# Optimization experiments

Hardware: AMD Instinct MI355X
Metric: run time of the kernel (lower is better)

Reference implementation:

```python
import jax, jax.numpy as jnp
import numpy as np

N_NODES = 100000
N_EDGES = 1600000
N_GRAPHS = 2048
HID = 64
IN_F = 14
N_CLS = 2
EPS = 1e-5


def _gcn_conv(x, row, col, w_edge, W, b, n_nodes):
    # PyG GCNConv with add_self_loops=True, normalize=True.
    xw = x @ W  # [N, out]
    # degree on target nodes, self-loop contributes weight 1
    deg = jnp.zeros((n_nodes,), x.dtype).at[col].add(w_edge) + 1.0
    dinv = deg ** -0.5
    norm = dinv[row] * w_edge * dinv[col]  # [E]
    out = jnp.zeros_like(xw).at[col].add(norm[:, None] * xw[row])
    out = out + (dinv * dinv)[:, None] * xw  # self-loop term
    return out + b


def _bn_relu(x, gamma, beta):
    mean = jnp.mean(x, axis=0)
    var = jnp.var(x, axis=0)  # biased, as PyTorch BN training normalization
    y = gamma * (x - mean) * jax.lax.rsqrt(var + EPS) + beta
    return jax.nn.relu(y)


def setup_inputs() -> dict:
    key = jax.random.key(0)
    ks = jax.random.split(key, 8)
    x = jax.random.normal(ks[0], (N_NODES, IN_F), dtype=jnp.float32)
    edge_index = jax.random.randint(ks[1], (2, N_EDGES), 0, N_NODES, dtype=jnp.int64)
    batch = jnp.sort(jax.random.randint(ks[2], (N_NODES,), 0, N_GRAPHS, dtype=jnp.int64))
    edge_weight = jnp.ones((N_EDGES,), dtype=jnp.float32)
    def lin(k, fi, fo):
        s = 1.0 / np.sqrt(fi)
        kw, kb = jax.random.split(k)
        return (jax.random.uniform(kw, (fi, fo), jnp.float32, -s, s),
                jax.random.uniform(kb, (fo,), jnp.float32, -s, s))
    W1, b1 = lin(ks[3], IN_F, HID)
    W2, b2 = lin(ks[4], HID, HID)
    W3, b3 = lin(ks[5], HID, HID)
    fcW, fcb = lin(ks[6], HID, N_CLS)
    g = jnp.ones((HID,), jnp.float32)
    z = jnp.zeros((HID,), jnp.float32)
    return {
        "x": x, "edge_index": edge_index, "batch": batch, "edge_weight": edge_weight,
        "W1": W1, "b1": b1, "W2": W2, "b2": b2, "W3": W3, "b3": b3,
        "g1": g, "bt1": z, "g2": g, "bt2": z, "g3": g, "bt3": z,
        "fcW": fcW, "fcb": fcb,
    }


def reference(x, edge_index, batch, edge_weight, W1, b1, W2, b2, W3, b3,
              g1, bt1, g2, bt2, g3, bt3, fcW, fcb):
    row, col = edge_index[0], edge_index[1]
    n = x.shape[0]
    h = _bn_relu(_gcn_conv(x, row, col, edge_weight, W1, b1, n), g1, bt1)
    h = _bn_relu(_gcn_conv(h, row, col, edge_weight, W2, b2, n), g2, bt2)
    h = _bn_relu(_gcn_conv(h, row, col, edge_weight, W3, b3, n), g3, bt3)
    node_embs = h  # dropout p=0 is identity
    graph_emb = jax.ops.segment_sum(node_embs, batch, num_segments=N_GRAPHS)
    out = graph_emb @ fcW + fcb
    return (out, node_embs, graph_emb)
```

## Files before the change

kernel.cpp:

```cpp
#include <hip/hip_runtime.h>
#include <hip/hip_fp16.h>

#define N_NODES 100000
#define N_EDGES 1600000
#define EMAX2   1700000
#define N_GRAPHS 2048
#define HID 64
#define IN_F 14
#define N_CLS 2
#define EPS 1e-5f

#define BSHIFT 9
#define NBUCK 196
#define ABLOCKS 256
#define CHUNK (N_EDGES / ABLOCKS)

#define NBLK2 128
#define NCHUNK2 ((N_NODES + NBLK2 - 1) / NBLK2)

typedef _Float16 half_t;
typedef _Float16 half8 __attribute__((ext_vector_type(8)));
typedef float f32x4 __attribute__((ext_vector_type(4)));

#define GSTRIDE ((size_t)N_NODES * 16)


__global__ __launch_bounds__(256) void histA_kernel(const int* __restrict__ col,
                                                    int* __restrict__ histG) {
    __shared__ int hl[NBUCK];
    for (int i = threadIdx.x; i < NBUCK; i += 256) hl[i] = 0;
    __syncthreads();
    int e0 = blockIdx.x * CHUNK;
    for (int e = e0 + threadIdx.x; e < e0 + CHUNK; e += 256)
        atomicAdd(&hl[col[e] >> BSHIFT], 1);
    __syncthreads();
    for (int i = threadIdx.x; i < NBUCK; i += 256)
        histG[i * ABLOCKS + blockIdx.x] = hl[i];
}

__global__ __launch_bounds__(256) void scanS1_kernel(const int* __restrict__ histG,
                                                     int* __restrict__ bsumA) {
    __shared__ int ls[256];
    ls[threadIdx.x] = histG[blockIdx.x * 256 + threadIdx.x];
    __syncthreads();
    for (int off = 128; off > 0; off >>= 1) {
        if (threadIdx.x < off) ls[threadIdx.x] += ls[threadIdx.x + off];
        __syncthreads();
    }
    if (threadIdx.x == 0) bsumA[blockIdx.x] = ls[0];
}

__global__ __launch_bounds__(512) void topscan_kernel(int* __restrict__ bsum, int nb) {
    __shared__ int ls[512];
    int t = threadIdx.x;
    int v = (t < nb) ? bsum[t] : 0;
    ls[t] = v;
    __syncthreads();
    for (int off = 1; off < 512; off <<= 1) {
        int x = ls[t];
        if (t >= off) x += ls[t - off];
        __syncthreads();
        ls[t] = x;
        __syncthreads();
    }
    if (t < nb) bsum[t] = ls[t] - v;
}

__global__ __launch_bounds__(256) void scanS3_kernel(int* __restrict__ histG,
                                                     const int* __restrict__ bsumA,
                                                     int* __restrict__ ptr) {
    __shared__ int ls[256];
    int idx = blockIdx.x * 256 + threadIdx.x;
    int v = histG[idx];
    ls[threadIdx.x] = v;
    __syncthreads();
    for (int off = 1; off < 256; off <<= 1) {
        int x = ls[threadIdx.x];
        if (threadIdx.x >= off) x += ls[threadIdx.x - off];
        __syncthreads();
        ls[threadIdx.x] = x;
        __syncthreads();
    }
    histG[idx] = ls[threadIdx.x] - v + bsumA[blockIdx.x];
    if (blockIdx.x == 0 && threadIdx.x == 0) ptr[N_NODES] = N_EDGES;
}

__global__ __launch_bounds__(256) void scatterA_kernel(const int* __restrict__ row,
                                                       const int* __restrict__ col,
                                                       const float* __restrict__ w,
                                                       const int* __restrict__ histG,
                                                       int2* __restrict__ EA) {
    __shared__ int cur[NBUCK];
    for (int i = threadIdx.x; i < NBUCK; i += 256)
        cur[i] = histG[i * ABLOCKS + blockIdx.x];
    __syncthreads();
    int e0 = blockIdx.x * CHUNK;
    for (int e = e0 + threadIdx.x; e < e0 + CHUNK; e += 256) {
        int c = col[e];
        int r = row[e];
        int fx = (int)__float2uint_rn(w[e] * 8192.0f);
        int pos = atomicAdd(&cur[c >> BSHIFT], 1);
        EA[pos] = make_int2(r, (fx << 17) | c);
    }
}

__global__ __launch_bounds__(256) void bucketA_kernel(const int2* __restrict__ EA,
                                                      const int* __restrict__ bsumA,
                                                      int* __restrict__ ptr,
                                                      float* __restrict__ dinv) {
    __shared__ int hist[512], wsum[512];
    int b = blockIdx.x;
    int beg = bsumA[b];
    int end = (b == NBUCK - 1) ? N_EDGES : bsumA[b + 1];
    int i0 = threadIdx.x, i1 = threadIdx.x + 256;
    hist[i0] = 0; hist[i1] = 0;
    wsum[i0] = 0; wsum[i1] = 0;
    __syncthreads();
    for (int e = beg + threadIdx.x; e < end; e += 256) {
        int2 ed = EA[e];
        int c9 = ed.y & 511;
        atomicAdd(&hist[c9], 1);
        atomicAdd(&wsum[c9], (int)((unsigned int)ed.y >> 17));
    }
    __syncthreads();
    int cnt0 = hist[i0], cnt1 = hist[i1];
    for (int off = 1; off < 512; off <<= 1) {
        int v0 = hist[i0], v1 = hist[i1];
        int a0 = (i0 >= off) ? hist[i0 - off] : 0;
        int a1 = (i1 >= off) ? hist[i1 - off] : 0;
        __syncthreads();
        hist[i0] = v0 + a0;
        hist[i1] = v1 + a1;
        __syncthreads();
    }
    int excl0 = hist[i0] - cnt0, excl1 = hist[i1] - cnt1;
    int col0 = (b << BSHIFT) + i0, col1 = (b << BSHIFT) + i1;
    if (col0 < N_NODES) {
        ptr[col0] = beg + excl0;
        dinv[col0] = rsqrtf(1.0f + (float)wsum[i0] * (1.0f / 8192.0f));
    }
    if (col1 < N_NODES) {
        ptr[col1] = beg + excl1;
        dinv[col1] = rsqrtf(1.0f + (float)wsum[i1] * (1.0f / 8192.0f));
    }
}


__global__ __launch_bounds__(256) void histD_kernel(const int* __restrict__ ptr,
                                                    int* __restrict__ histD) {
    __shared__ int hl[2048];
    for (int i = threadIdx.x; i < 2048; i += 256) hl[i] = 0;
    __syncthreads();
    int n0 = blockIdx.x * NCHUNK2;
    int n1 = n0 + NCHUNK2; if (n1 > N_NODES) n1 = N_NODES;
    for (int n = n0 + threadIdx.x; n < n1; n += 256) {
        int d = ptr[n + 1] - ptr[n];
        if (d > 255) d = 255;
        atomicAdd(&hl[((threadIdx.x & 7) << 8) + d], 1);
    }
    __syncthreads();
    int s = 0;
#pragma unroll
    for (int c = 0; c < 8; c++) s += hl[(c << 8) + threadIdx.x];
    histD[threadIdx.x * NBLK2 + blockIdx.x] = s;
}

__global__ __launch_bounds__(128) void scanD1_kernel(const int* __restrict__ histD,
                                                     int* __restrict__ rowTot) {
    __shared__ int ls[128];
    ls[threadIdx.x] = histD[blockIdx.x * NBLK2 + threadIdx.x];
    __syncthreads();
    for (int off = 64; off > 0; off >>= 1) {
        if (threadIdx.x < off) ls[threadIdx.x] += ls[threadIdx.x + off];
        __syncthreads();
    }
    if (threadIdx.x == 0) rowTot[blockIdx.x] = ls[0];
}

__global__ __launch_bounds__(256) void topscanD_kernel(const int* __restrict__ rowTot,
                                                       int* __restrict__ nodeExcl,
                                                       int* __restrict__ edgeExcl,
                                                       int* __restrict__ ptrS) {
    __shared__ int a[256], b[256];
    int t = threadIdx.x;
    int cnt = rowTot[t];
    int dpad = (t + 1) & ~1;
    int ec = cnt * dpad;
    a[t] = cnt; b[t] = ec;
    __syncthreads();
    for (int off = 1; off < 256; off <<= 1) {
        int va = a[t], vb = b[t];
        if (t >= off) { va += a[t - off]; vb += b[t - off]; }
        __syncthreads();
        a[t] = va; b[t] = vb;
        __syncthreads();
    }
    nodeExcl[t] = a[t] - cnt;
    edgeExcl[t] = b[t] - ec;
    if (t == 255) ptrS[N_NODES] = b[255];
}

__global__ __launch_bounds__(128) void scanD3_kernel(int* __restrict__ histD,
                                                     const int* __restrict__ nodeExcl) {
    __shared__ int ls[128];
    int idx = blockIdx.x * NBLK2 + threadIdx.x;
    int v = histD[idx];
    ls[threadIdx.x] = v;
    __syncthreads();
    for (int off = 1; off < 128; off <<= 1) {
        int x = ls[threadIdx.x];
        if (threadIdx.x >= off) x += ls[threadIdx.x - off];
        __syncthreads();
        ls[threadIdx.x] = x;
        __syncthreads();
    }
    histD[idx] = ls[threadIdx.x] - v + nodeExcl[blockIdx.x];
}

__global__ __launch_bounds__(256) void scatterD_kernel(const int* __restrict__ ptr,
                                                       const int* __restrict__ histD,
                                                       const int* __restrict__ nodeExcl,
                                                       const int* __restrict__ edgeExcl,
                                                       int* __restrict__ perm,
                                                       int* __restrict__ ptrS,
                                                       int* __restrict__ newbase) {
    __shared__ int cur[256];
    cur[threadIdx.x] = histD[threadIdx.x * NBLK2 + blockIdx.x];
    __syncthreads();
    int n0 = blockIdx.x * NCHUNK2;
    int n1 = n0 + NCHUNK2; if (n1 > N_NODES) n1 = N_NODES;
    for (int n = n0 + threadIdx.x; n < n1; n += 256) {
        int d = ptr[n + 1] - ptr[n];
        if (d > 255) d = 255;
        int dpad = (d + 1) & ~1;
        int pos = atomicAdd(&cur[d], 1);
        int ebase = edgeExcl[d] + (pos - nodeExcl[d]) * dpad;
        perm[pos] = n;
        ptrS[pos] = ebase;
        newbase[n] = ebase;
    }
}

__global__ __launch_bounds__(256) void bucketB_kernel(const int2* __restrict__ EA,
                                                      const int* __restrict__ bsumA,
                                                      const int* __restrict__ newbase,
                                                      const float* __restrict__ dinv,
                                                      unsigned int* __restrict__ srcoff,
                                                      half_t* __restrict__ normh) {
    __shared__ int cur[512];
    int b = blockIdx.x;
    int beg = bsumA[b];
    int end = (b == NBUCK - 1) ? N_EDGES : bsumA[b + 1];
    int i0 = threadIdx.x, i1 = threadIdx.x + 256;
    int col0 = (b << BSHIFT) + i0, col1 = (b << BSHIFT) + i1;
    cur[i0] = (col0 < N_NODES) ? newbase[col0] : 0;
    cur[i1] = (col1 < N_NODES) ? newbase[col1] : 0;
    __syncthreads();
    for (int e = beg + threadIdx.x; e < end; e += 256) {
        int2 ed = EA[e];
        int c = ed.y & 0x1ffff;
        float w = (float)((unsigned int)ed.y >> 17) * (1.0f / 8192.0f);
        float nrm = dinv[ed.x] * w * dinv[c];
        int pos = atomicAdd(&cur[c & 511], 1);
        srcoff[pos] = (unsigned int)ed.x << 5;
        normh[pos] = (half_t)nrm;
    }
}


template <int K>
__global__ __launch_bounds__(256) void gemm_kernel(const float* __restrict__ h,
                                                   const float* __restrict__ W,
                                                   half_t* __restrict__ xw, int n_nodes) {
    int f = threadIdx.x & 63;
    float wcol[K];
#pragma unroll
    for (int k = 0; k < K; k++) wcol[k] = W[k * HID + f];
    half_t* xg = xw + (size_t)(f >> 4) * GSTRIDE + (f & 15);
    int wave = (blockIdx.x * blockDim.x + threadIdx.x) >> 6;
    int nwaves = (gridDim.x * blockDim.x) >> 6;
    for (int n = wave; n < n_nodes; n += nwaves) {
        const float* hr = h + (size_t)n * K;
        float acc = 0.f;
#pragma unroll
        for (int k = 0; k < K; k++) acc += hr[k] * wcol[k];
        xg[(size_t)n * 16] = (half_t)acc;
    }
}

__global__ __launch_bounds__(256) void gemm_bn_mfma_kernel(const half_t* __restrict__ h,
                                                           const float* __restrict__ W,
                                                           const float* __restrict__ stats,
                                                           const float* __restrict__ gamma,
                                                           const float* __restrict__ beta,
                                                           half_t* __restrict__ xw, int n_nodes) {
    __shared__ float sc_s[HID], sh_s[HID];
    if (threadIdx.x < 64) {
        float mean = stats[threadIdx.x] * (1.0f / N_NODES);
        float var = stats[64 + threadIdx.x] * (1.0f / N_NODES) - mean * mean;
        float sc = gamma[threadIdx.x] * rsqrtf(var + EPS);
        sc_s[threadIdx.x] = sc;
        sh_s[threadIdx.x] = beta[threadIdx.x] - mean * sc;
    }
    __syncthreads();
    int lane = threadIdx.x & 63;
    int col16 = lane & 15;
    int quad = lane >> 4;

    float scA[2][8], shA[2][8];
#pragma unroll
    for (int kh = 0; kh < 2; kh++)
#pragma unroll
        for (int j = 0; j < 8; j++) {
            int k = kh * 32 + quad * 8 + j;
            scA[kh][j] = sc_s[k];
            shA[kh][j] = sh_s[k];
        }

    half8 bfrag[4][2];
#pragma unroll
    for (int t = 0; t < 4; t++)
#pragma unroll
        for (int kh = 0; kh < 2; kh++)
#pragma unroll
            for (int j = 0; j < 8; j++) {
                int k = kh * 32 + quad * 8 + j;
                bfrag[t][kh][j] = (half_t)W[k * HID + t * 16 + col16];
            }

    int wave = (blockIdx.x * blockDim.x + threadIdx.x) >> 6;
    int nwaves = (gridDim.x * blockDim.x) >> 6;
    int ntiles = n_nodes >> 4;
    for (int tIdx = wave; tIdx < ntiles; tIdx += nwaves) {
        int n0 = tIdx << 4;
        half8 afrag[2];
#pragma unroll
        for (int kh = 0; kh < 2; kh++) {
            int k0 = kh * 32 + quad * 8;
            const half_t* hp = h + (size_t)(k0 >> 4) * GSTRIDE
                                 + (size_t)(n0 + col16) * 16 + (k0 & 15);
            half8 raw = *(const half8*)hp;
#pragma unroll
            for (int j = 0; j < 8; j++) {
                float v = (float)raw[j] * scA[kh][j] + shA[kh][j];
                afrag[kh][j] = (half_t)fmaxf(v, 0.f);
            }
        }
        f32x4 acc[4];
#pragma unroll
        for (int t = 0; t < 4; t++) {
            f32x4 z = {0.f, 0.f, 0.f, 0.f};
            acc[t] = __builtin_amdgcn_mfma_f32_16x16x32_f16(afrag[0], bfrag[t][0], z, 0, 0, 0);
            acc[t] = __builtin_amdgcn_mfma_f32_16x16x32_f16(afrag[1], bfrag[t][1], acc[t], 0, 0, 0);
        }
#pragma unroll
        for (int t = 0; t < 4; t++) {
            half_t* xg = xw + (size_t)t * GSTRIDE;
#pragma unroll
            for (int r = 0; r < 4; r++) {
                int rowi = n0 + quad * 4 + r;
                xg[(size_t)rowi * 16 + col16] = (half_t)acc[t][r];
            }
        }
    }
}

__global__ __launch_bounds__(256) void gather_stats_kernel(const int* __restrict__ ptrS,
                                                           const int* __restrict__ perm,
                                                           const unsigned int* __restrict__ srcoff,
                                                           const unsigned int* __restrict__ normu,
                                                           const half_t* __restrict__ xw,
                                                           const float* __restrict__ dinv,
                                                           const float* __restrict__ b,
                                                           half_t* __restrict__ hp,
                                                           float* __restrict__ stats,
                                                           int n_nodes) {
    int g = (blockIdx.x & 7) >> 1;
    int grank = ((blockIdx.x >> 3) << 1) | (blockIdx.x & 1);
    int lane16 = threadIdx.x & 15;
    int quadLocal = threadIdx.x >> 4;
    int quadId = grank * 16 + quadLocal;
    int nquads = (gridDim.x >> 2) * 16;

    const half_t* xg = xw + (size_t)g * GSTRIDE;
    const char* xgc = (const char*)xg;
    unsigned int loff = (unsigned int)(lane16 * 2);
    half_t* hpg = hp + (size_t)g * GSTRIDE;
    int f = g * 16 + lane16;
    float bf = b[f];
    int base = ((threadIdx.x & 63) >> 4) * 16;

    float s = 0.f, s2 = 0.f;

    int i = quadId;
    int node = 0, beg = 0, c = 0;
    int ev = 0, nv = 0;
    if (i < n_nodes) {
        node = perm[i];
        beg = ptrS[i];
        c = ptrS[i + 1] - beg;
        int m = (c > 16) ? 16 : c;
        if (lane16 < m) ev = (int)srcoff[beg + lane16];
        if (lane16 < (m >> 1)) nv = (int)normu[(beg >> 1) + lane16];
    }

    while (i < n_nodes) {
        int inext = i + nquads;
        int node2 = 0, beg2 = 0, c2 = 0;
        if (inext < n_nodes) {
            node2 = perm[inext];
            beg2 = ptrS[inext];
            c2 = ptrS[inext + 1] - beg2;
        }
        float selfv = (float)xg[(size_t)node * 16 + lane16];
        float di = dinv[node];

        __half2 acc0 = __float2half2_rn(0.f);
        __half2 acc1 = __float2half2_rn(0.f);
        for (int j0 = 0; j0 < c; j0 += 16) {
            int m = c - j0;
            if (m > 16) m = 16;
            int pairs = m >> 1;
            int ev2 = 0, nv2 = 0;
            int j1 = j0 + 16;
            if (j1 < c) {
                int m2 = c - j1;
                if (m2 > 16) m2 = 16;
                if (lane16 < m2) ev2 = (int)srcoff[beg + j1 + lane16];
                if (lane16 < (m2 >> 1)) nv2 = (int)normu[((beg + j1) >> 1) + lane16];
            }
            int p = 0;
            for (; p + 2 <= pairs; p += 2) {
                unsigned int u0 = (unsigned int)__shfl(ev, base + 2 * p);
                unsigned int u1 = (unsigned int)__shfl(ev, base + 2 * p + 1);
                unsigned int u2 = (unsigned int)__shfl(ev, base + 2 * p + 2);
                unsigned int u3 = (unsigned int)__shfl(ev, base + 2 * p + 3);
                unsigned int nd0 = (unsigned int)__shfl(nv, base + p);
                unsigned int nd1 = (unsigned int)__shfl(nv, base + p + 1);
                __half h0 = *(const __half*)(xgc + (u0 + loff));
                __half h1 = *(const __half*)(xgc + (u1 + loff));
                __half h2 = *(const __half*)(xgc + (u2 + loff));
                __half h3 = *(const __half*)(xgc + (u3 + loff));
                __half2 n01 = *(__half2*)&nd0;
                __half2 n23 = *(__half2*)&nd1;
                acc0 = __hfma2(n01, __halves2half2(h0, h1), acc0);
                acc1 = __hfma2(n23, __halves2half2(h2, h3), acc1);
            }
            if (p < pairs) {
                unsigned int u0 = (unsigned int)__shfl(ev, base + 2 * p);
                unsigned int u1 = (unsigned int)__shfl(ev, base + 2 * p + 1);
                unsigned int nd0 = (unsigned int)__shfl(nv, base + p);
                __half h0 = *(const __half*)(xgc + (u0 + loff));
                __half h1 = *(const __half*)(xgc + (u1 + loff));
                __half2 n01 = *(__half2*)&nd0;
                acc0 = __hfma2(n01, __halves2half2(h0, h1), acc0);
            }
            ev = ev2; nv = nv2;
        }
        if (inext < n_nodes) {
            int m = (c2 > 16) ? 16 : c2;
            ev = (lane16 < m) ? (int)srcoff[beg2 + lane16] : 0;
            nv = (lane16 < (m >> 1)) ? (int)normu[(beg2 >> 1) + lane16] : 0;
        }

        float accf = (__low2float(acc0) + __high2float(acc0))
                   + (__low2float(acc1) + __high2float(acc1));
        float v = accf + di * di * selfv + bf;
        hpg[(size_t)node * 16 + lane16] = (half_t)v;
        s += v;
        s2 += v * v;

        i = inext; node = node2; beg = beg2; c = c2;
    }
    __shared__ float ls[256], ls2[256];
    ls[threadIdx.x] = s;
    ls2[threadIdx.x] = s2;
    __syncthreads();
    if (threadIdx.x < 16) {
        float a = 0.f, aa = 0.f;
#pragma unroll
        for (int k = 0; k < 16; k++) {
            a += ls[k * 16 + threadIdx.x];
            aa += ls2[k * 16 + threadIdx.x];
        }
        atomicAdd(&stats[g * 16 + threadIdx.x], a);
        atomicAdd(&stats[64 + g * 16 + threadIdx.x], aa);
    }
}

__global__ __launch_bounds__(256) void bn_relu_seg_kernel(const half_t* __restrict__ hpl,
                                                          float* __restrict__ h3,
                                                          const float* __restrict__ stats,
                                                          const float* __restrict__ gamma,
                                                          const float* __restrict__ beta,
                                                          const int* __restrict__ batch,
                                                          float* __restrict__ gemb,
                                                          int n_nodes) {
    int g = blockIdx.x * blockDim.x + threadIdx.x;
    int f = g & 63;
    int wave = g >> 6;
    int nwaves = (gridDim.x * blockDim.x) >> 6;
    int chunk = (n_nodes + nwaves - 1) / nwaves;
    int n0 = wave * chunk;
    int n1 = n0 + chunk;
    if (n1 > n_nodes) n1 = n_nodes;
    if (n0 >= n_nodes) return;
    float mean = stats[f] * (1.0f / N_NODES);
    float var = stats[64 + f] * (1.0f / N_NODES) - mean * mean;
    float sc = gamma[f] * rsqrtf(var + EPS);
    float sh = beta[f] - mean * sc;
    const half_t* hg = hpl + (size_t)(f >> 4) * GSTRIDE + (f & 15);
    int curg = batch[n0];
    float racc = 0.f;
    for (int n = n0; n < n1; n++) {
        int bg = batch[n];
        if (bg != curg) {
            atomicAdd(&gemb[(size_t)curg * HID + f], racc);
            racc = 0.f;
            curg = bg;
        }
        float v = (float)hg[(size_t)n * 16] * sc + sh;
        v = fmaxf(v, 0.f);
        h3[(size_t)n * HID + f] = v;
        racc += v;
    }
    atomicAdd(&gemb[(size_t)curg * HID + f], racc);
}

__global__ __launch_bounds__(256) void final_kernel(const float* __restrict__ gemb,
                                                    const float* __restrict__ fcW,
                                                    const float* __restrict__ fcb,
                                                    float* __restrict__ out) {
    int g = blockIdx.x * blockDim.x + threadIdx.x;
    if (g >= N_GRAPHS * N_CLS) return;
    int gr = g >> 1, c = g & 1;
    float acc = fcb[c];
#pragma unroll
    for (int k = 0; k < HID; k++) acc += gemb[gr * HID + k] * fcW[k * N_CLS + c];
    out[g] = acc;
}


extern "C" void kernel_launch(void* const* d_in, const int* in_sizes, int n_in,
                              void* d_out, int out_size, void* d_ws, size_t ws_size,
                              hipStream_t stream) {
    const float* x    = (const float*)d_in[0];
    const int*   ei   = (const int*)d_in[1];
    const int*   batch= (const int*)d_in[2];
    const float* ew   = (const float*)d_in[3];
    const float* W1   = (const float*)d_in[4];
    const float* b1   = (const float*)d_in[5];
    const float* W2   = (const float*)d_in[6];
    const float* b2   = (const float*)d_in[7];
    const float* W3   = (const float*)d_in[8];
    const float* b3   = (const float*)d_in[9];
    const float* g1   = (const float*)d_in[10];
    const float* bt1  = (const float*)d_in[11];
    const float* g2   = (const float*)d_in[12];
    const float* bt2  = (const float*)d_in[13];
    const float* g3   = (const float*)d_in[14];
    const float* bt3  = (const float*)d_in[15];
    const float* fcW  = (const float*)d_in[16];
    const float* fcb  = (const float*)d_in[17];

    const int* row = ei;
    const int* col = ei + N_EDGES;

    float* out_head  = (float*)d_out;
    float* node_embs = out_head + N_GRAPHS * N_CLS;
    float* gemb      = node_embs + (size_t)N_NODES * HID;

    char* bse = (char*)d_ws;
    half_t* xwh = (half_t*)bse;
    char* r1 = bse + (size_t)N_NODES * HID * 2;
    int2*   EA  = (int2*)r1;
    half_t* hpl = (half_t*)r1;
    char* r2 = r1 + (size_t)N_NODES * HID * 2;
    unsigned int* srcoff = (unsigned int*)r2;
    half_t* normh = (half_t*)(srcoff + EMAX2);
    char* r3 = r2 + (size_t)EMAX2 * 6;
    float* dinv  = (float*)r3;
    float* stats3 = dinv + N_NODES;
    int*   ptr   = (int*)(stats3 + 384);
    int*   histG = ptr + N_NODES + 1;
    int*   bsumA = histG + NBUCK * ABLOCKS;
    int*   histD = bsumA + NBUCK + 4;
    int*   rowTot = histD + 256 * NBLK2;
    int*   nodeExcl = rowTot + 256;
    int*   edgeExcl = nodeExcl + 256;
    int*   perm   = edgeExcl + 256;
    int*   newbase= perm + N_NODES;
    int*   ptrS   = newbase + N_NODES;

    const int B   = 256;
    const int gGS = 1024;
    const int gGA = 2048;

    hipMemsetAsync(srcoff, 0, (size_t)EMAX2 * 6, stream);
    hipMemsetAsync(stats3, 0, 384 * sizeof(float), stream);
    hipMemsetAsync(gemb, 0, (size_t)N_GRAPHS * HID * sizeof(float), stream);

    histA_kernel<<<ABLOCKS, B, 0, stream>>>(col, histG);
    scanS1_kernel<<<NBUCK, B, 0, stream>>>(histG, bsumA);
    topscan_kernel<<<1, 512, 0, stream>>>(bsumA, NBUCK);
    scanS3_kernel<<<NBUCK, B, 0, stream>>>(histG, bsumA, ptr);
    scatterA_kernel<<<ABLOCKS, B, 0, stream>>>(row, col, ew, histG, EA);
    bucketA_kernel<<<NBUCK, B, 0, stream>>>(EA, bsumA, ptr, dinv);

    histD_kernel<<<NBLK2, B, 0, stream>>>(ptr, histD);
    scanD1_kernel<<<256, 128, 0, stream>>>(histD, rowTot);
    topscanD_kernel<<<1, 256, 0, stream>>>(rowTot, nodeExcl, edgeExcl, ptrS);
    scanD3_kernel<<<256, 128, 0, stream>>>(histD, nodeExcl);
    scatterD_kernel<<<NBLK2, B, 0, stream>>>(ptr, histD, nodeExcl, edgeExcl,
                                             perm, ptrS, newbase);
    bucketB_kernel<<<NBUCK, B, 0, stream>>>(EA, bsumA, newbase, dinv, srcoff, normh);

    float* h3 = node_embs;

    gemm_kernel<IN_F><<<gGS, B, 0, stream>>>(x, W1, xwh, N_NODES);
    gather_stats_kernel<<<gGA, B, 0, stream>>>(ptrS, perm, srcoff,
                                               (const unsigned int*)normh, xwh,
                                               dinv, b1, hpl, stats3, N_NODES);

    gemm_bn_mfma_kernel<<<gGS, B, 0, stream>>>(hpl, W2, stats3, g1, bt1, xwh, N_NODES);
    gather_stats_kernel<<<gGA, B, 0, stream>>>(ptrS, perm, srcoff,
                                               (const unsigned int*)normh, xwh,
                                               dinv, b2, hpl, stats3 + 128, N_NODES);

    gemm_bn_mfma_kernel<<<gGS, B, 0, stream>>>(hpl, W3, stats3 + 128, g2, bt2, xwh, N_NODES);
    gather_stats_kernel<<<gGA, B, 0, stream>>>(ptrS, perm, srcoff,
                                               (const unsigned int*)normh, xwh,
                                               dinv, b3, hpl, stats3 + 256, N_NODES);

    bn_relu_seg_kernel<<<gGS, B, 0, stream>>>(hpl, h3, stats3 + 256, g3, bt3,
                                              batch, gemb, N_NODES);

    final_kernel<<<(N_GRAPHS * N_CLS + B - 1) / B, B, 0, stream>>>(gemb, fcW, fcb, out_head);
}
```

Measured before the change: 407.6 us.

## Pad CSR edge lists to multiples of four and load indices as vectors

Per-node edge segments are now padded to a multiple of four instead of two, with the edge buffer capacity raised to match. The aggregation kernel then drops the cooperative shuffle-based broadcast of source offsets and norms, and has each lane read them directly with uint4/uint2 vector loads. This removes shuffle instructions and the prefetch logic, but increases padded edge storage and issues redundant broadcast loads across the 16 lanes of each node group. It also loses the software prefetch of the next node's indices.

```diff
diff --git a/kernel.cpp b/kernel.cpp
--- a/kernel.cpp
+++ b/kernel.cpp
@@ -3,7 +3,7 @@
 
 #define N_NODES 100000
 #define N_EDGES 1600000
-#define EMAX2   1700000
+#define EMAX2   2000000
 #define N_GRAPHS 2048
 #define HID 64
 #define IN_F 14
@@ -184,7 +184,7 @@
     __shared__ int a[256], b[256];
     int t = threadIdx.x;
     int cnt = rowTot[t];
-    int dpad = (t + 1) & ~1;
+    int dpad = (t + 3) & ~3;
     int ec = cnt * dpad;
     a[t] = cnt; b[t] = ec;
     __syncthreads();
@@ -232,7 +232,7 @@
     for (int n = n0 + threadIdx.x; n < n1; n += 256) {
         int d = ptr[n + 1] - ptr[n];
         if (d > 255) d = 255;
-        int dpad = (d + 1) & ~1;
+        int dpad = (d + 3) & ~3;
         int pos = atomicAdd(&cur[d], 1);
         int ebase = edgeExcl[d] + (pos - nodeExcl[d]) * dpad;
         perm[pos] = n;
@@ -388,22 +388,16 @@
     half_t* hpg = hp + (size_t)g * GSTRIDE;
     int f = g * 16 + lane16;
     float bf = b[f];
-    int base = ((threadIdx.x & 63) >> 4) * 16;
 
     float s = 0.f, s2 = 0.f;
 
     int i = quadId;
     int node = 0, beg = 0, c = 0;
-    int ev = 0, nv = 0;
     if (i < n_nodes) {
         node = perm[i];
         beg = ptrS[i];
         c = ptrS[i + 1] - beg;
-        int m = (c > 16) ? 16 : c;
-        if (lane16 < m) ev = (int)srcoff[beg + lane16];
-        if (lane16 < (m >> 1)) nv = (int)normu[(beg >> 1) + lane16];
-    }
-
+    }
     while (i < n_nodes) {
         int inext = i + nquads;
         int node2 = 0, beg2 = 0, c2 = 0;
@@ -417,52 +411,38 @@
 
         __half2 acc0 = __float2half2_rn(0.f);
         __half2 acc1 = __float2half2_rn(0.f);
-        for (int j0 = 0; j0 < c; j0 += 16) {
-            int m = c - j0;
-            if (m > 16) m = 16;
-            int pairs = m >> 1;
-            int ev2 = 0, nv2 = 0;
-            int j1 = j0 + 16;
-            if (j1 < c) {
-                int m2 = c - j1;
-                if (m2 > 16) m2 = 16;
-                if (lane16 < m2) ev2 = (int)srcoff[beg + j1 + lane16];
-                if (lane16 < (m2 >> 1)) nv2 = (int)normu[((beg + j1) >> 1) + lane16];
-            }
-            int p = 0;
-            for (; p + 2 <= pairs; p += 2) {
-                unsigned int u0 = (unsigned int)__shfl(ev, base + 2 * p);
-                unsigned int u1 = (unsigned int)__shfl(ev, base + 2 * p + 1);
-                unsigned int u2 = (unsigned int)__shfl(ev, base + 2 * p + 2);
-                unsigned int u3 = (unsigned int)__shfl(ev, base + 2 * p + 3);
-                unsigned int nd0 = (unsigned int)__shfl(nv, base + p);
-                unsigned int nd1 = (unsigned int)__shfl(nv, base + p + 1);
-                __half h0 = *(const __half*)(xgc + (u0 + loff));
-                __half h1 = *(const __half*)(xgc + (u1 + loff));
-                __half h2 = *(const __half*)(xgc + (u2 + loff));
-                __half h3 = *(const __half*)(xgc + (u3 + loff));
-                __half2 n01 = *(__half2*)&nd0;
-                __half2 n23 = *(__half2*)&nd1;
-                acc0 = __hfma2(n01, __halves2half2(h0, h1), acc0);
-                acc1 = __hfma2(n23, __halves2half2(h2, h3), acc1);
-            }
-            if (p < pairs) {
-                unsigned int u0 = (unsigned int)__shfl(ev, base + 2 * p);
-                unsigned int u1 = (unsigned int)__shfl(ev, base + 2 * p + 1);
-                unsigned int nd0 = (unsigned int)__shfl(nv, base + p);
-                __half h0 = *(const __half*)(xgc + (u0 + loff));
-                __half h1 = *(const __half*)(xgc + (u1 + loff));
-                __half2 n01 = *(__half2*)&nd0;
-                acc0 = __hfma2(n01, __halves2half2(h0, h1), acc0);
-            }
-            ev = ev2; nv = nv2;
-        }
-        if (inext < n_nodes) {
-            int m = (c2 > 16) ? 16 : c2;
-            ev = (lane16 < m) ? (int)srcoff[beg2 + lane16] : 0;
-            nv = (lane16 < (m >> 1)) ? (int)normu[(beg2 >> 1) + lane16] : 0;
-        }
-
+        const uint4* up = (const uint4*)(srcoff + beg);
+        const uint2* np = (const uint2*)(normu + (beg >> 1));
+        int q4 = c >> 2;
+        int j = 0;
+        for (; j + 2 <= q4; j += 2) {
+            uint4 ua = up[j];
+            uint4 ub = up[j + 1];
+            uint2 na = np[j];
+            uint2 nb = np[j + 1];
+            __half ha0 = *(const __half*)(xgc + (ua.x + loff));
+            __half ha1 = *(const __half*)(xgc + (ua.y + loff));
+            __half ha2 = *(const __half*)(xgc + (ua.z + loff));
+            __half ha3 = *(const __half*)(xgc + (ua.w + loff));
+            __half hb0 = *(const __half*)(xgc + (ub.x + loff));
+            __half hb1 = *(const __half*)(xgc + (ub.y + loff));
+            __half hb2 = *(const __half*)(xgc + (ub.z + loff));
+            __half hb3 = *(const __half*)(xgc + (ub.w + loff));
+            acc0 = __hfma2(*(const __half2*)&na.x, __halves2half2(ha0, ha1), acc0);
+            acc1 = __hfma2(*(const __half2*)&na.y, __halves2half2(ha2, ha3), acc1);
+            acc0 = __hfma2(*(const __half2*)&nb.x, __halves2half2(hb0, hb1), acc0);
+            acc1 = __hfma2(*(const __half2*)&nb.y, __halves2half2(hb2, hb3), acc1);
+        }
+        if (j < q4) {
+            uint4 ua = up[j];
+            uint2 na = np[j];
+            __half ha0 = *(const __half*)(xgc + (ua.x + loff));
+            __half ha1 = *(const __half*)(xgc + (ua.y + loff));
+            __half ha2 = *(const __half*)(xgc + (ua.z + loff));
+            __half ha3 = *(const __half*)(xgc + (ua.w + loff));
+            acc0 = __hfma2(*(const __half2*)&na.x, __halves2half2(ha0, ha1), acc0);
+            acc1 = __hfma2(*(const __half2*)&na.y, __halves2half2(ha2, ha3), acc1);
+        }
         float accf = (__low2float(acc0) + __high2float(acc0))
                    + (__low2float(acc1) + __high2float(acc1));
         float v = accf + di * di * selfv + bf;
```

After: 435.1 us. 6.7% more time.
